# Kernel tuning notes

Measured on AMD Instinct MI355X. Metric: run time of the kernel, lower is better.

The kernel has to match this reference:

```python
import jax, jax.numpy as jnp
import numpy as np

B, S, WIN5, E, H = 64, 2048, 50, 128, 256


def setup_inputs() -> dict:
    key = jax.random.key(0)
    ks = jax.random.split(key, 11)
    return {
        "prev_window": jax.random.normal(ks[0], (B, S, WIN5), dtype=jnp.float32),
        "W_emb": jax.random.normal(ks[1], (E, WIN5), dtype=jnp.float32) * 0.1,
        "b_emb": jax.random.normal(ks[2], (E,), dtype=jnp.float32) * 0.1,
        "W_ih": jax.random.normal(ks[3], (4 * H, E), dtype=jnp.float32) * 0.05,
        "W_hh": jax.random.normal(ks[4], (4 * H, H), dtype=jnp.float32) * 0.05,
        "b_ih": jax.random.normal(ks[5], (4 * H,), dtype=jnp.float32) * 0.05,
        "b_hh": jax.random.normal(ks[6], (4 * H,), dtype=jnp.float32) * 0.05,
        "W_out": jax.random.normal(ks[7], (1, H), dtype=jnp.float32) * 0.1,
        "b_out": jax.random.normal(ks[8], (1,), dtype=jnp.float32) * 0.1,
        "h0": jax.random.uniform(ks[9], (B, H), dtype=jnp.float32),
        "c0": jax.random.uniform(ks[10], (B, H), dtype=jnp.float32),
    }


def reference(prev_window, W_emb, b_emb, W_ih, W_hh, b_ih, b_hh, W_out, b_out, h0, c0):
    # embedding: [B, S, E], relu(Linear)
    emb = jax.nn.relu(jnp.einsum("bsw,ew->bse", prev_window, W_emb) + b_emb)
    # precompute input projections for all steps: [S, B, 4H]
    x_gates = jnp.einsum("bse,ge->sbg", emb, W_ih) + b_ih + b_hh

    def step(carry, xg):
        h, c = carry
        gates = xg + h @ W_hh.T  # [B, 4H]
        i, f, g, o = jnp.split(gates, 4, axis=-1)
        i = jax.nn.sigmoid(i)
        f = jax.nn.sigmoid(f)
        g = jnp.tanh(g)
        o = jax.nn.sigmoid(o)
        c = f * c + i * g
        h = o * jnp.tanh(c)
        return (h, c), h

    _, hs = jax.lax.scan(step, (h0, c0), x_gates)  # hs: [S, B, H]
    # dropout rate is 0.0 -> identity
    y = jax.nn.sigmoid(jnp.einsum("sbh,oh->sbo", hs, W_out) + b_out)  # [S, B, 1]
    return y
```

## Files before the change

kernel.cpp:

```cpp
#include <hip/hip_runtime.h>
#include <hip/hip_bf16.h>

#define B_ 64
#define S_ 2048
#define W_ 50
#define E_ 128
#define H_ 256
#define G_ 1024

typedef unsigned short u16;
typedef unsigned int u32;
typedef unsigned char u8;
typedef unsigned int v4u __attribute__((ext_vector_type(4)));
typedef __attribute__((ext_vector_type(8))) short short8;
typedef __attribute__((ext_vector_type(4))) float f32x4;

__device__ int g_mode;
__device__ u16 g_WA[E_ * G_];
__device__ float g_bias[G_];
__device__ u32 g_Wi8[G_ * 64];
__device__ float g_wscale[G_];
__device__ u16 g_xg[(size_t)B_ * S_ * G_];
__device__ float g_hs[(size_t)B_ * S_ * H_];

__device__ __forceinline__ float b2f(u16 u) {
    union { u32 i; float f; } v;
    v.i = ((u32)u) << 16;
    return v.f;
}
__device__ __forceinline__ u16 f2b(float f) {
    __hip_bfloat16 h = __float2bfloat16(f);
    return *reinterpret_cast<u16*>(&h);
}
__device__ __forceinline__ float ldin(int mode, const void* p, size_t i) {
    return mode ? ((const float*)p)[i] : b2f(((const u16*)p)[i]);
}
__device__ __forceinline__ float clamp30(float x) {
    return fminf(fmaxf(x, -30.0f), 30.0f);
}
__device__ __forceinline__ float sigmoidf_(float x) { return 1.0f / (1.0f + __expf(-x)); }
__device__ __forceinline__ float tanhf_(float x) {
    float e = __expf(2.0f * x);
    return 1.0f - 2.0f / (e + 1.0f);
}
__device__ __forceinline__ float fastrcp(float x) {
    float r;
    asm("v_rcp_f32 %0, %1" : "=v"(r) : "v"(x));
    return r;
}
__device__ __forceinline__ float fsig(float x) { return fastrcp(1.0f + __expf(-x)); }
__device__ __forceinline__ float ftanh(float x) {
    return fmaf(-2.0f, fastrcp(1.0f + __expf(2.0f * x)), 1.0f);
}
__device__ __forceinline__ int dppadd1(int x) {
    return x + __builtin_amdgcn_update_dpp(0, x, 0xB1, 0xF, 0xF, true);
}
__device__ __forceinline__ int dot4i8(u32 a, u32 b, int acc) {
#if __has_builtin(__builtin_amdgcn_sdot4)
    return __builtin_amdgcn_sdot4(a, b, acc, false);
#else
    acc += (int)(signed char)(a)       * (int)(signed char)(b);
    acc += (int)(signed char)(a >> 8)  * (int)(signed char)(b >> 8);
    acc += (int)(signed char)(a >> 16) * (int)(signed char)(b >> 16);
    acc += (int)(signed char)(a >> 24) * (int)(signed char)(b >> 24);
    return acc;
#endif
}

__global__ void sniff_kernel(const u16* __restrict__ wemb) {
    int sane = 0;
    for (int i = 0; i < 2048; ++i) {
        int ex = (wemb[i] >> 7) & 0xFF;
        if (ex == 0 || (ex >= 96 && ex <= 143)) ++sane;
    }
    g_mode = (sane >= 1900) ? 0 : 1;
}

__global__ __launch_bounds__(256) void prep_wa(const void* __restrict__ src) {
    const int mode = g_mode;
    int i = blockIdx.x * 256 + threadIdx.x;
    int j = i & 7, l = (i >> 3) & 63, ks = (i >> 9) & 3, ct = i >> 11;
    int c = ct * 16 + (l & 15);
    int e = ks * 32 + (l >> 4) * 8 + j;
    int row = ((c & 3) << 8) + (c >> 2);
    g_WA[i] = f2b(ldin(mode, src, (size_t)row * E_ + e));
}

__global__ __launch_bounds__(256) void prep_wi8(const void* __restrict__ src,
                                                const void* __restrict__ bih,
                                                const void* __restrict__ bhh) {
    const int mode = g_mode;
    int c = blockIdx.x * 256 + threadIdx.x;
    int row = ((c & 3) << 8) + (c >> 2);
    g_bias[c] = ldin(mode, bih, row) + ldin(mode, bhh, row);
    const size_t base = (size_t)row * H_;
    float m = 0.0f;
    for (int k = 0; k < H_; ++k) m = fmaxf(m, fabsf(ldin(mode, src, base + k)));
    float inv = (m > 0.0f) ? 127.0f / m : 0.0f;
    g_wscale[c] = m / (127.0f * 127.0f);
    for (int j = 0; j < 64; ++j) {
        u32 pk = 0;
#pragma unroll
        for (int i = 0; i < 4; ++i) {
            int q = (int)rintf(ldin(mode, src, base + 4 * j + i) * inv);
            q = max(-127, min(127, q));
            pk |= ((u32)(q & 0xff)) << (8 * i);
        }
        g_Wi8[(size_t)(c >> 2) * 256 + j * 4 + (c & 3)] = pk;
    }
}

__global__ __launch_bounds__(256) void xg_mfma(const void* __restrict__ pw,
                                               const void* __restrict__ Wemb,
                                               const void* __restrict__ bemb) {
    const int mode = g_mode;
    const int t = threadIdx.x;
    const int m0 = blockIdx.x * 64;
    __shared__ float pwS[64][W_ + 2];
    __shared__ float Wl[E_ * 51];
    __shared__ __align__(16) u16 embL[64][136];

    for (int i = t; i < E_ * W_; i += 256) {
        int e = i / W_, w = i - e * W_;
        Wl[e * 51 + w] = ldin(mode, Wemb, i);
    }
    for (int i = t; i < 64 * W_; i += 256) {
        int r = i / W_, w = i - r * W_;
        pwS[r][w] = ldin(mode, pw, (size_t)(m0 + r) * W_ + w);
    }
    __syncthreads();

    {
        const int e = t & 127;
        float wreg[W_];
#pragma unroll
        for (int w = 0; w < W_; ++w) wreg[w] = Wl[e * 51 + w];
        const float bb = ldin(mode, bemb, e);
#pragma unroll
        for (int i = 0; i < 32; ++i) {
            const int r = i * 2 + (t >> 7);
            float a = bb;
#pragma unroll
            for (int w = 0; w < W_; ++w) a = fmaf(pwS[r][w], wreg[w], a);
            embL[r][e] = f2b(fmaxf(a, 0.0f));
        }
    }
    __syncthreads();

    const int l = t & 63;
    const int wv = t >> 6;
    const int lr = l & 15;
    const int lh = l >> 4;
    short8 Bf[4][4];
#pragma unroll
    for (int rg = 0; rg < 4; ++rg)
#pragma unroll
        for (int ks = 0; ks < 4; ++ks)
            Bf[rg][ks] = *(const short8*)&embL[rg * 16 + lr][ks * 32 + lh * 8];

    const short8* wa = (const short8*)g_WA;
#pragma unroll 2
    for (int tt = 0; tt < 16; ++tt) {
        const int ct = wv * 16 + tt;
        const int cbase = ct * 16;
        const short8 A0 = wa[(ct * 4 + 0) * 64 + l];
        const short8 A1 = wa[(ct * 4 + 1) * 64 + l];
        const short8 A2 = wa[(ct * 4 + 2) * 64 + l];
        const short8 A3 = wa[(ct * 4 + 3) * 64 + l];
        const float4 bv = *(const float4*)(g_bias + cbase + 4 * lh);
#pragma unroll
        for (int rg = 0; rg < 4; ++rg) {
            f32x4 acc = {bv.x, bv.y, bv.z, bv.w};
            acc = __builtin_amdgcn_mfma_f32_16x16x32_bf16(A0, Bf[rg][0], acc, 0, 0, 0);
            acc = __builtin_amdgcn_mfma_f32_16x16x32_bf16(A1, Bf[rg][1], acc, 0, 0, 0);
            acc = __builtin_amdgcn_mfma_f32_16x16x32_bf16(A2, Bf[rg][2], acc, 0, 0, 0);
            acc = __builtin_amdgcn_mfma_f32_16x16x32_bf16(A3, Bf[rg][3], acc, 0, 0, 0);
            u32 p0 = (u32)f2b(acc[0]) | ((u32)f2b(acc[1]) << 16);
            u32 p1 = (u32)f2b(acc[2]) | ((u32)f2b(acc[3]) << 16);
            uint2 pv; pv.x = p0; pv.y = p1;
            *(uint2*)(g_xg + (size_t)(m0 + rg * 16 + lr) * G_ + cbase + 4 * lh) = pv;
        }
    }
}

__global__ __launch_bounds__(512)
__attribute__((amdgpu_waves_per_eu(2, 2)))
void lstm_split(const void* __restrict__ h0, const void* __restrict__ c0) {
    const int mode = g_mode;
    const int t = threadIdx.x;
    const int b = blockIdx.x;
    const int u = t >> 1;
    const int half = t & 1;

    __shared__ __align__(16) u32 h8[2][H_ / 4];

    v4u W00, W01, W02, W03, W04, W05, W06, W07, W08, W09, W10, W11, W12, W13, W14, W15;
    v4u W16, W17, W18, W19, W20, W21, W22, W23, W24, W25, W26, W27, W28, W29, W30, W31;
    {
        const u32* wp = g_Wi8 + (size_t)t * 128;
        asm volatile(
            "global_load_dwordx4 %0, %16, off\n\t"
            "global_load_dwordx4 %1, %16, off offset:16\n\t"
            "global_load_dwordx4 %2, %16, off offset:32\n\t"
            "global_load_dwordx4 %3, %16, off offset:48\n\t"
            "global_load_dwordx4 %4, %16, off offset:64\n\t"
            "global_load_dwordx4 %5, %16, off offset:80\n\t"
            "global_load_dwordx4 %6, %16, off offset:96\n\t"
            "global_load_dwordx4 %7, %16, off offset:112\n\t"
            "global_load_dwordx4 %8, %16, off offset:128\n\t"
            "global_load_dwordx4 %9, %16, off offset:144\n\t"
            "global_load_dwordx4 %10, %16, off offset:160\n\t"
            "global_load_dwordx4 %11, %16, off offset:176\n\t"
            "global_load_dwordx4 %12, %16, off offset:192\n\t"
            "global_load_dwordx4 %13, %16, off offset:208\n\t"
            "global_load_dwordx4 %14, %16, off offset:224\n\t"
            "global_load_dwordx4 %15, %16, off offset:240\n\t"
            "s_waitcnt vmcnt(0)"
            : "=&v"(W00), "=&v"(W01), "=&v"(W02), "=&v"(W03),
              "=&v"(W04), "=&v"(W05), "=&v"(W06), "=&v"(W07),
              "=&v"(W08), "=&v"(W09), "=&v"(W10), "=&v"(W11),
              "=&v"(W12), "=&v"(W13), "=&v"(W14), "=&v"(W15)
            : "v"(wp));
        asm volatile(
            "global_load_dwordx4 %0, %16, off offset:256\n\t"
            "global_load_dwordx4 %1, %16, off offset:272\n\t"
            "global_load_dwordx4 %2, %16, off offset:288\n\t"
            "global_load_dwordx4 %3, %16, off offset:304\n\t"
            "global_load_dwordx4 %4, %16, off offset:320\n\t"
            "global_load_dwordx4 %5, %16, off offset:336\n\t"
            "global_load_dwordx4 %6, %16, off offset:352\n\t"
            "global_load_dwordx4 %7, %16, off offset:368\n\t"
            "global_load_dwordx4 %8, %16, off offset:384\n\t"
            "global_load_dwordx4 %9, %16, off offset:400\n\t"
            "global_load_dwordx4 %10, %16, off offset:416\n\t"
            "global_load_dwordx4 %11, %16, off offset:432\n\t"
            "global_load_dwordx4 %12, %16, off offset:448\n\t"
            "global_load_dwordx4 %13, %16, off offset:464\n\t"
            "global_load_dwordx4 %14, %16, off offset:480\n\t"
            "global_load_dwordx4 %15, %16, off offset:496\n\t"
            "s_waitcnt vmcnt(0)"
            : "=&v"(W16), "=&v"(W17), "=&v"(W18), "=&v"(W19),
              "=&v"(W20), "=&v"(W21), "=&v"(W22), "=&v"(W23),
              "=&v"(W24), "=&v"(W25), "=&v"(W26), "=&v"(W27),
              "=&v"(W28), "=&v"(W29), "=&v"(W30), "=&v"(W31)
            : "v"(wp));
    }

    const float4 wsc4 = *(const float4*)(g_wscale + 4 * u);
    float c_reg = (half == 0) ? ldin(mode, c0, (size_t)b * H_ + u) : 0.0f;

    if (t < H_ / 4) {
        u32 pk = 0;
#pragma unroll
        for (int i = 0; i < 4; ++i) {
            float h = ldin(mode, h0, (size_t)b * H_ + 4 * t + i);
            int q = (int)rintf(fminf(fmaxf(h, -1.0f), 1.0f) * 127.0f);
            pk |= ((u32)(q & 0xff)) << (8 * i);
        }
        h8[0][t] = pk;
    }
    const u16* xp = g_xg + (size_t)b * S_ * G_ + 4 * u;
    float* hsp = g_hs + (size_t)b * S_ * H_ + u;

    ushort4 xq[4];
#pragma unroll
    for (int e = 0; e < 4; ++e)
        xq[e] = *(const ushort4*)(xp + (size_t)e * G_);

    asm volatile("s_waitcnt lgkmcnt(0)\n\t"
                 "s_barrier" ::: "memory");

#define DOTG(HV, WA, WB, WC, WD)                                              \
            ai = dot4i8(HV.x, WA.x, ai); af = dot4i8(HV.x, WA.y, af);         \
            ag = dot4i8(HV.x, WA.z, ag); ao = dot4i8(HV.x, WA.w, ao);         \
            ai = dot4i8(HV.y, WB.x, ai); af = dot4i8(HV.y, WB.y, af);         \
            ag = dot4i8(HV.y, WB.z, ag); ao = dot4i8(HV.y, WB.w, ao);         \
            ai = dot4i8(HV.z, WC.x, ai); af = dot4i8(HV.z, WC.y, af);         \
            ag = dot4i8(HV.z, WC.z, ag); ao = dot4i8(HV.z, WC.w, ao);         \
            ai = dot4i8(HV.w, WD.x, ai); af = dot4i8(HV.w, WD.y, af);         \
            ag = dot4i8(HV.w, WD.z, ag); ao = dot4i8(HV.w, WD.w, ao);

    for (int s0 = 0; s0 < S_; s0 += 4) {
#pragma unroll
        for (int e = 0; e < 4; ++e) {
            const int s = s0 + e;
            const ushort4 xv = xq[e];
            const int sn = (s + 4 < S_) ? s + 4 : s;
            xq[e] = *(const ushort4*)(xp + (size_t)sn * G_);

            const uint4* hp = (const uint4*)h8[s & 1] + half * 8;
            uint4 h0v = hp[0], h1v = hp[1], h2v = hp[2], h3v = hp[3];
            uint4 h4v = hp[4], h5v = hp[5], h6v = hp[6], h7v = hp[7];

            int ai = 0, af = 0, ag = 0, ao = 0;
            DOTG(h0v, W00, W01, W02, W03)
            DOTG(h1v, W04, W05, W06, W07)
            DOTG(h2v, W08, W09, W10, W11)
            DOTG(h3v, W12, W13, W14, W15)
            DOTG(h4v, W16, W17, W18, W19)
            DOTG(h5v, W20, W21, W22, W23)
            DOTG(h6v, W24, W25, W26, W27)
            DOTG(h7v, W28, W29, W30, W31)

            ai = dppadd1(ai);
            af = dppadd1(af);
            ag = dppadd1(ag);
            ao = dppadd1(ao);

            if (half == 0) {
                float gi = (float)ai * wsc4.x + b2f(xv.x);
                float gf = (float)af * wsc4.y + b2f(xv.y);
                float gg = (float)ag * wsc4.z + b2f(xv.z);
                float go = (float)ao * wsc4.w + b2f(xv.w);
                float ii = fsig(gi);
                float ff = fsig(gf);
                float gv = ftanh(gg);
                float oo = fsig(go);
                c_reg = fmaf(ff, c_reg, ii * gv);
                float h = oo * ftanh(c_reg);
                int q = (int)rintf(h * 127.0f) & 0xff;
                ((u8*)h8[(s + 1) & 1])[u] = (u8)q;
                hsp[(size_t)s * H_] = h;
            }
            asm volatile("s_waitcnt lgkmcnt(0)\n\t"
                         "s_barrier" ::: "memory");
        }
    }
#undef DOTG
}

__global__ __launch_bounds__(256) void head_kernel(const void* __restrict__ Wout,
                                                   const void* __restrict__ bout,
                                                   void* __restrict__ yv) {
    const int mode = g_mode;
    const int t = threadIdx.x;
    const int idx = blockIdx.x * 4 + (t >> 6);
    const int l = t & 63;
    const int s = idx >> 6, b = idx & 63;
    const float* hb = g_hs + ((size_t)b * S_ + s) * H_ + 4 * l;
    float4 hv = *(const float4*)hb;
    float p = hv.x * ldin(mode, Wout, 4 * l + 0)
            + hv.y * ldin(mode, Wout, 4 * l + 1)
            + hv.z * ldin(mode, Wout, 4 * l + 2)
            + hv.w * ldin(mode, Wout, 4 * l + 3);
#pragma unroll
    for (int off = 32; off > 0; off >>= 1) p += __shfl_down(p, off, 64);
    if (l == 0) {
        float yf = sigmoidf_(clamp30(p + ldin(mode, bout, 0)));
        if (mode) ((float*)yv)[(size_t)s * B_ + b] = yf;
        else      ((u16*)yv)[(size_t)s * B_ + b] = f2b(yf);
    }
}

extern "C" void kernel_launch(void* const* d_in, const int* in_sizes, int n_in,
                              void* d_out, int out_size, void* d_ws, size_t ws_size,
                              hipStream_t stream) {
    const void* pw   = d_in[0];
    const void* Wemb = d_in[1];
    const void* bemb = d_in[2];
    const void* Wih  = d_in[3];
    const void* Whh  = d_in[4];
    const void* bih  = d_in[5];
    const void* bhh  = d_in[6];
    const void* Wout = d_in[7];
    const void* bout = d_in[8];
    const void* h0   = d_in[9];
    const void* c0   = d_in[10];
    void* y = d_out;
    (void)d_ws; (void)ws_size;

    sniff_kernel<<<1, 1, 0, stream>>>((const u16*)Wemb);
    prep_wa<<<(E_ * G_) / 256, 256, 0, stream>>>(Wih);
    prep_wi8<<<G_ / 256, 256, 0, stream>>>(Whh, bih, bhh);
    xg_mfma<<<(B_ * S_) / 64, 256, 0, stream>>>(pw, Wemb, bemb);
    lstm_split<<<B_, 512, 0, stream>>>(h0, c0);
    head_kernel<<<(S_ * B_) / 4, 256, 0, stream>>>(Wout, bout, y);
}
```

Before: 2.090 ms.

## Process two batch rows per LSTM block, sharing register-resident weights and barriers

Each lstm_split block now advances two batch elements together, reusing the int8 recurrent weights held in registers for both, and uses half as many blocks. Both elements' gate dot products and cell updates run between one barrier per timestep, so the per-step sync and latency cost is spread over twice the work. The trade-off is twice the serial compute per step inside each block and only 32 blocks running, which leaves many CUs idle. Register pressure also rises from the second cell state and the extra prefetch buffers. The per-step xg prefetch now only runs on half==0 threads.

New measurement: 4.274 ms. 105% more time.

```diff
diff --git a/kernel.cpp b/kernel.cpp
--- a/kernel.cpp
+++ b/kernel.cpp
@@ -188,11 +188,12 @@
 void lstm_split(const void* __restrict__ h0, const void* __restrict__ c0) {
     const int mode = g_mode;
     const int t = threadIdx.x;
-    const int b = blockIdx.x;
+    const int b0 = blockIdx.x * 2;
+    const int b1 = b0 + 1;
     const int u = t >> 1;
     const int half = t & 1;
 
-    __shared__ __align__(16) u32 h8[2][H_ / 4];
+    __shared__ __align__(16) u32 h8[2][2][H_ / 4];
 
     v4u W00, W01, W02, W03, W04, W05, W06, W07, W08, W09, W10, W11, W12, W13, W14, W15;
     v4u W16, W17, W18, W19, W20, W21, W22, W23, W24, W25, W26, W27, W28, W29, W30, W31;
@@ -247,25 +248,34 @@
     }
 
     const float4 wsc4 = *(const float4*)(g_wscale + 4 * u);
-    float c_reg = (half == 0) ? ldin(mode, c0, (size_t)b * H_ + u) : 0.0f;
-
-    if (t < H_ / 4) {
+    float cr0 = 0.0f, cr1 = 0.0f;
+    if (half == 0) {
+        cr0 = ldin(mode, c0, (size_t)b0 * H_ + u);
+        cr1 = ldin(mode, c0, (size_t)b1 * H_ + u);
+    }
+
+    if (t < 128) {
+        const int bi = t >> 6, tt = t & 63;
         u32 pk = 0;
 #pragma unroll
         for (int i = 0; i < 4; ++i) {
-            float h = ldin(mode, h0, (size_t)b * H_ + 4 * t + i);
+            float h = ldin(mode, h0, (size_t)(b0 + bi) * H_ + 4 * tt + i);
             int q = (int)rintf(fminf(fmaxf(h, -1.0f), 1.0f) * 127.0f);
             pk |= ((u32)(q & 0xff)) << (8 * i);
         }
-        h8[0][t] = pk;
-    }
-    const u16* xp = g_xg + (size_t)b * S_ * G_ + 4 * u;
-    float* hsp = g_hs + (size_t)b * S_ * H_ + u;
-
-    ushort4 xq[4];
-#pragma unroll
-    for (int e = 0; e < 4; ++e)
-        xq[e] = *(const ushort4*)(xp + (size_t)e * G_);
+        h8[bi][0][tt] = pk;
+    }
+    const u16* xp0 = g_xg + (size_t)b0 * S_ * G_ + 4 * u;
+    const u16* xp1 = g_xg + (size_t)b1 * S_ * G_ + 4 * u;
+    float* hsp0 = g_hs + (size_t)b0 * S_ * H_ + u;
+    float* hsp1 = g_hs + (size_t)b1 * S_ * H_ + u;
+
+    ushort4 xq0[4], xq1[4];
+#pragma unroll
+    for (int e = 0; e < 4; ++e) {
+        xq0[e] = *(const ushort4*)(xp0 + (size_t)e * G_);
+        xq1[e] = *(const ushort4*)(xp1 + (size_t)e * G_);
+    }
 
     asm volatile("s_waitcnt lgkmcnt(0)\n\t"
                  "s_barrier" ::: "memory");
@@ -280,52 +290,55 @@
             ai = dot4i8(HV.w, WD.x, ai); af = dot4i8(HV.w, WD.y, af);         \
             ag = dot4i8(HV.w, WD.z, ag); ao = dot4i8(HV.w, WD.w, ao);
 
+#define BSTEP(BI, CREG, XQ, XP, HSP, E, S, SN)                                \
+    {                                                                         \
+        const uint4* hp = (const uint4*)h8[BI][(S) & 1] + half * 8;           \
+        uint4 h0v = hp[0], h1v = hp[1], h2v = hp[2], h3v = hp[3];             \
+        uint4 h4v = hp[4], h5v = hp[5], h6v = hp[6], h7v = hp[7];             \
+        int ai = 0, af = 0, ag = 0, ao = 0;                                   \
+        DOTG(h0v, W00, W01, W02, W03)                                         \
+        DOTG(h1v, W04, W05, W06, W07)                                         \
+        DOTG(h2v, W08, W09, W10, W11)                                         \
+        DOTG(h3v, W12, W13, W14, W15)                                         \
+        DOTG(h4v, W16, W17, W18, W19)                                         \
+        DOTG(h5v, W20, W21, W22, W23)                                         \
+        DOTG(h6v, W24, W25, W26, W27)                                         \
+        DOTG(h7v, W28, W29, W30, W31)                                         \
+        ai = dppadd1(ai);                                                     \
+        af = dppadd1(af);                                                     \
+        ag = dppadd1(ag);                                                     \
+        ao = dppadd1(ao);                                                     \
+        if (half == 0) {                                                      \
+            const ushort4 xv = XQ[E];                                         \
+            XQ[E] = *(const ushort4*)(XP + (size_t)(SN) * G_);                \
+            float gi = (float)ai * wsc4.x + b2f(xv.x);                        \
+            float gf = (float)af * wsc4.y + b2f(xv.y);                        \
+            float gg = (float)ag * wsc4.z + b2f(xv.z);                        \
+            float go = (float)ao * wsc4.w + b2f(xv.w);                        \
+            float ii = fsig(gi);                                              \
+            float ff = fsig(gf);                                              \
+            float gv = ftanh(gg);                                             \
+            float oo = fsig(go);                                              \
+            CREG = fmaf(ff, CREG, ii * gv);                                   \
+            float h = oo * ftanh(CREG);                                       \
+            int q = (int)rintf(h * 127.0f) & 0xff;                            \
+            ((u8*)h8[BI][((S) + 1) & 1])[u] = (u8)q;                          \
+            HSP[(size_t)(S) * H_] = h;                                        \
+        }                                                                     \
+    }
+
     for (int s0 = 0; s0 < S_; s0 += 4) {
 #pragma unroll
         for (int e = 0; e < 4; ++e) {
             const int s = s0 + e;
-            const ushort4 xv = xq[e];
             const int sn = (s + 4 < S_) ? s + 4 : s;
-            xq[e] = *(const ushort4*)(xp + (size_t)sn * G_);
-
-            const uint4* hp = (const uint4*)h8[s & 1] + half * 8;
-            uint4 h0v = hp[0], h1v = hp[1], h2v = hp[2], h3v = hp[3];
-            uint4 h4v = hp[4], h5v = hp[5], h6v = hp[6], h7v = hp[7];
-
-            int ai = 0, af = 0, ag = 0, ao = 0;
-            DOTG(h0v, W00, W01, W02, W03)
-            DOTG(h1v, W04, W05, W06, W07)
-            DOTG(h2v, W08, W09, W10, W11)
-            DOTG(h3v, W12, W13, W14, W15)
-            DOTG(h4v, W16, W17, W18, W19)
-            DOTG(h5v, W20, W21, W22, W23)
-            DOTG(h6v, W24, W25, W26, W27)
-            DOTG(h7v, W28, W29, W30, W31)
-
-            ai = dppadd1(ai);
-            af = dppadd1(af);
-            ag = dppadd1(ag);
-            ao = dppadd1(ao);
-
-            if (half == 0) {
-                float gi = (float)ai * wsc4.x + b2f(xv.x);
-                float gf = (float)af * wsc4.y + b2f(xv.y);
-                float gg = (float)ag * wsc4.z + b2f(xv.z);
-                float go = (float)ao * wsc4.w + b2f(xv.w);
-                float ii = fsig(gi);
-                float ff = fsig(gf);
-                float gv = ftanh(gg);
-                float oo = fsig(go);
-                c_reg = fmaf(ff, c_reg, ii * gv);
-                float h = oo * ftanh(c_reg);
-                int q = (int)rintf(h * 127.0f) & 0xff;
-                ((u8*)h8[(s + 1) & 1])[u] = (u8)q;
-                hsp[(size_t)s * H_] = h;
-            }
+            BSTEP(0, cr0, xq0, xp0, hsp0, e, s, sn)
+            BSTEP(1, cr1, xq1, xp1, hsp1, e, s, sn)
             asm volatile("s_waitcnt lgkmcnt(0)\n\t"
                          "s_barrier" ::: "memory");
         }
     }
+#undef BSTEP
 #undef DOTG
 }
 
@@ -373,6 +386,6 @@
     prep_wa<<<(E_ * G_) / 256, 256, 0, stream>>>(Wih);
     prep_wi8<<<G_ / 256, 256, 0, stream>>>(Whh, bih, bhh);
     xg_mfma<<<(B_ * S_) / 64, 256, 0, stream>>>(pw, Wemb, bemb);
-    lstm_split<<<B_, 512, 0, stream>>>(h0, c0);
+    lstm_split<<<B_ / 2, 512, 0, stream>>>(h0, c0);
     head_kernel<<<(S_ * B_) / 4, 256, 0, stream>>>(Wout, bout, y);
 }
```
